# Kernel tuning notes

Measured on AMD Instinct MI355X. Metric: run time of the kernel, lower is better.

## Reference

```python
import jax, jax.numpy as jnp
import numpy as np

TOPK, NPRO, NALP, NADS = 13, 31, 24, 37
ALPHA, BETA, EPS = 1.0, 6.0, 1e-9
BS, NA, NM = 32, 8400, 64
IMG = 640.0


def _make_boxes(key, shape, img=IMG):
    k1, k2 = jax.random.split(key)
    cxy = jax.random.uniform(k1, shape[:-1] + (2,), minval=0.0, maxval=img)
    wh = jax.random.uniform(k2, shape[:-1] + (2,), minval=10.0, maxval=120.0)
    return jnp.concatenate([cxy - wh / 2, cxy + wh / 2], axis=-1)


def setup_inputs() -> dict:
    key = jax.random.key(0)
    ks = jax.random.split(key, 12)
    pd_pro_scores = jax.random.uniform(ks[0], (BS, NA, NPRO))
    pd_alp_scores = jax.random.uniform(ks[1], (BS, NA, NALP))
    pd_ads_scores = jax.random.uniform(ks[2], (5, BS, NA, NADS))
    pd_bboxes = _make_boxes(ks[3], (BS, NA, 4))
    pd_corners = jax.random.uniform(ks[4], (BS, NA, 8), maxval=IMG)
    anc_points = jax.random.uniform(ks[5], (NA, 2), maxval=IMG)
    gt_pro = jax.random.randint(ks[6], (BS, NM, 1), 0, NPRO, dtype=jnp.int32)
    gt_alp = jax.random.randint(ks[7], (BS, NM, 1), 0, NALP, dtype=jnp.int32)
    gt_ads = jax.random.randint(ks[8], (BS, NM, 5), 0, NADS, dtype=jnp.int32)
    gt_bboxes = _make_boxes(ks[9], (BS, NM, 4))
    gt_corners = jax.random.uniform(ks[10], (BS, NM, 8), maxval=IMG)
    nvalid = jax.random.randint(ks[11], (BS,), NM // 2, NM + 1)
    mask_gt = (jnp.arange(NM)[None, :] < nvalid[:, None]).astype(jnp.float32)[..., None]
    return {"pd_pro_scores": pd_pro_scores, "pd_alp_scores": pd_alp_scores,
            "pd_ads_scores": pd_ads_scores, "pd_bboxes": pd_bboxes,
            "pd_corners": pd_corners, "anc_points": anc_points,
            "gt_pro": gt_pro, "gt_alp": gt_alp, "gt_ads": gt_ads,
            "gt_bboxes": gt_bboxes, "gt_corners": gt_corners, "mask_gt": mask_gt}


def _iou(gt, pd):
    # gt: (bs, nm, 4) xyxy; pd: (bs, na, 4) xyxy -> (bs, nm, na)
    g, p = gt[:, :, None, :], pd[:, None, :, :]
    lt = jnp.maximum(g[..., :2], p[..., :2])
    rb = jnp.minimum(g[..., 2:], p[..., 2:])
    inter = jnp.clip(rb - lt, 0).prod(-1)
    a1 = jnp.clip(g[..., 2:] - g[..., :2], 0).prod(-1)
    a2 = jnp.clip(p[..., 2:] - p[..., :2], 0).prod(-1)
    return inter / (a1 + a2 - inter + EPS)


def reference(pd_pro_scores, pd_alp_scores, pd_ads_scores, pd_bboxes, pd_corners,
              anc_points, gt_pro, gt_alp, gt_ads, gt_bboxes, gt_corners, mask_gt):
    bs, na = pd_pro_scores.shape[:2]
    nm = gt_bboxes.shape[1]
    b = jnp.arange(bs)[:, None]

    # --- get_box_metrics ---
    labels = gt_pro[..., 0].astype(jnp.int32)                       # (bs, nm)
    bbox_scores = pd_pro_scores.transpose(0, 2, 1)[b, labels]       # (bs, nm, na)
    overlaps = _iou(gt_bboxes, pd_bboxes)                           # (bs, nm, na)
    align = (bbox_scores ** ALPHA) * (overlaps ** BETA)

    # --- select_candidates_in_gts ---
    xy = anc_points[None, None]                                     # (1,1,na,2)
    d_lt = xy - gt_bboxes[:, :, None, :2]
    d_rb = gt_bboxes[:, :, None, 2:] - xy
    mask_in = (jnp.minimum(d_lt, d_rb).min(-1) > EPS).astype(align.dtype)

    # --- select_topk_candidates ---
    metrics = align * mask_in
    _, tidx = jax.lax.top_k(metrics, TOPK)                          # (bs, nm, topk)
    valid = mask_gt[..., 0] > 0                                     # (bs, nm)
    tidx = jnp.where(valid[..., None], tidx, 0)
    rows = jnp.arange(bs * nm)[:, None]
    counts = jnp.zeros((bs * nm, na), jnp.int32).at[rows, tidx.reshape(bs * nm, TOPK)].add(1)
    counts = counts.reshape(bs, nm, na)
    is_in_topk = jnp.where(counts > 1, 0, counts).astype(metrics.dtype)
    mask_pos = is_in_topk * mask_in * mask_gt                       # (bs, nm, na)

    # --- select_highest_overlaps ---
    fg_mask = mask_pos.sum(-2)                                      # (bs, na)
    multi = fg_mask > 1
    max_idx = overlaps.argmax(1)                                    # (bs, na)
    is_max = (jnp.arange(nm)[None, :, None] == max_idx[:, None, :]).astype(mask_pos.dtype)
    mask_pos = jnp.where(multi[:, None, :], is_max, mask_pos)
    fg_mask = mask_pos.sum(-2)
    target_gt_idx = mask_pos.argmax(-2)                             # (bs, na)

    # --- get_targets ---
    target_pro = jnp.maximum(gt_pro[..., 0].astype(jnp.int32)[b, target_gt_idx], 0)
    target_alp = jnp.maximum(gt_alp[..., 0].astype(jnp.int32)[b, target_gt_idx], 0)
    target_ads = jnp.maximum(gt_ads.astype(jnp.int32)[b, target_gt_idx], 0)   # (bs, na, 5)
    target_ad0_4 = jnp.moveaxis(target_ads, -1, 0)                  # (5, bs, na)
    target_bboxes = gt_bboxes[b, target_gt_idx]                     # (bs, na, 4)
    target_corners = gt_corners[b, target_gt_idx]                   # (bs, na, 8)

    fg = (fg_mask > 0).astype(jnp.float32)                          # (bs, na)
    pro_scores = jax.nn.one_hot(target_pro, NPRO, dtype=jnp.float32) * fg[..., None]
    alp_scores = jax.nn.one_hot(target_alp, NALP, dtype=jnp.float32) * fg[..., None]
    ads_scores = jax.nn.one_hot(target_ad0_4, NADS, dtype=jnp.float32) * fg[None, :, :, None]

    # --- normalization of pro scores ---
    align = align * mask_pos
    pos_align = align.max(-1, keepdims=True)                        # (bs, nm, 1)
    pos_ov = (overlaps * mask_pos).max(-1, keepdims=True)           # (bs, nm, 1)
    norm = (align * pos_ov / (pos_align + EPS)).max(-2)[..., None]  # (bs, na, 1)
    pro_scores = pro_scores * norm

    return (target_pro, target_alp, target_ad0_4, target_bboxes, target_corners,
            pro_scores, alp_scores, ads_scores, fg_mask > 0)
```

## Files before the change

### kernel.cpp

```cpp
#include <hip/hip_runtime.h>
#include <cstdint>
#include <cstddef>

#define BS 32
#define NA 8400
#define NM 64
#define NPRO 31
#define NALP 24
#define NADS 37
#define TOPK 13
#define FEPS 1e-9f
#define WORDS 264
#define CAP 512
#define TL 16

#define OFF0 0L
#define OFF1 268800L
#define OFF2 537600L
#define OFF3 1881600L
#define OFF4 2956800L
#define OFF5 5107200L
#define OFF6 13440000L
#define OFF7 19891200L
#define OFF8 69619200L

__device__ __forceinline__ float iou1(float4 g, float ga, float4 p, float pa) {
  float iw = fmaxf(fminf(g.z, p.z) - fmaxf(g.x, p.x), 0.f);
  float ih = fmaxf(fminf(g.w, p.w) - fmaxf(g.y, p.y), 0.f);
  float inter = iw * ih;
  return inter / (ga + pa - inter + FEPS);
}

__global__ __launch_bounds__(256) void kA(
    const float* __restrict__ pro, const float* __restrict__ pd_bb,
    const float* __restrict__ anc, const int* __restrict__ gt_pro,
    const float* __restrict__ gt_bb, const float* __restrict__ mask_gt,
    short* __restrict__ tlist, unsigned* __restrict__ posA,
    unsigned* __restrict__ posO)
{
  __shared__ unsigned s_in[WORDS];
  __shared__ unsigned s_pos[WORDS];
  __shared__ float s_cv[CAP];
  __shared__ int   s_ci[CAP];
  __shared__ int   s_cnt;

  const int bm = blockIdx.x;
  const int b = bm >> 6;
  const int tid = threadIdx.x;
  const int lane = tid & 63;

  if (tid == 0) { posA[bm] = 0u; posO[bm] = 0u; s_cnt = 0; }

  short* tl = tlist + bm * TL;
  if (!(mask_gt[bm] > 0.f)) {
    if (tid == 0) tl[0] = 0;
    return;
  }
  __syncthreads();

  const float4 g = *(const float4*)(gt_bb + (size_t)bm * 4);
  const int label = gt_pro[bm];
  const float ga = fmaxf(g.z - g.x, 0.f) * fmaxf(g.w - g.y, 0.f);
  const float* pb = pd_bb + (size_t)b * NA * 4;
  const float* ps = pro + (size_t)b * NA * NPRO + label;

  for (int j = 0; j < (NA + 255) / 256; j++) {
    const int a = j * 256 + tid;
    bool inb = false, posb = false; float met = 0.f;
    if (a < NA) {
      float2 ap = *(const float2*)(anc + 2 * a);
      float din = fminf(fminf(ap.x - g.x, ap.y - g.y), fminf(g.z - ap.x, g.w - ap.y));
      if (din > FEPS) {
        inb = true;
        float4 p = *(const float4*)(pb + (size_t)a * 4);
        float pa = fmaxf(p.z - p.x, 0.f) * fmaxf(p.w - p.y, 0.f);
        float iou = iou1(g, ga, p, pa);
        float i2 = iou * iou;
        met = ps[(size_t)a * NPRO] * (i2 * i2 * i2);
        posb = met > 0.f;
      }
    }
    unsigned long long bin  = __ballot(inb);
    unsigned long long bpos = __ballot(posb);
    if (lane == 0) {
      int w0 = (j << 3) + ((tid >> 6) << 1);
      s_in[w0]      = (unsigned)bin;
      s_in[w0 + 1]  = (unsigned)(bin >> 32);
      s_pos[w0]     = (unsigned)bpos;
      s_pos[w0 + 1] = (unsigned)(bpos >> 32);
    }
    if (bpos) {
      int base = 0;
      if (lane == 0) base = atomicAdd(&s_cnt, __popcll(bpos));
      base = __shfl(base, 0);
      if (posb) {
        int idx = base + __popcll(bpos & ((1ull << lane) - 1ull));
        if (idx < CAP) { s_cv[idx] = met; s_ci[idx] = a; }
      }
    }
  }
  __syncthreads();

  const int P = min(s_cnt, CAP);
  if (tid < 64) {
    float lv[8]; int li[8];
#pragma unroll
    for (int e = 0; e < 8; e++) {
      int p = tid + e * 64;
      bool ok = p < P;
      lv[e] = ok ? s_cv[p] : -1.f;
      li[e] = ok ? s_ci[p] : NA;
    }
    const int nsel = min(P, TOPK);
    for (int k = 0; k < nsel; k++) {
      float bv = -1.f; int bi = NA;
#pragma unroll
      for (int e = 0; e < 8; e++)
        if (lv[e] > bv || (lv[e] == bv && li[e] < bi)) { bv = lv[e]; bi = li[e]; }
      for (int s = 1; s < 64; s <<= 1) {
        float ov = __shfl_xor(bv, s);
        int   oi = __shfl_xor(bi, s);
        if (ov > bv || (ov == bv && oi < bi)) { bv = ov; bi = oi; }
      }
#pragma unroll
      for (int e = 0; e < 8; e++) if (li[e] == bi) lv[e] = -1.f;
      if (tid == 0) tl[1 + k] = (short)bi;
    }
    if (tid == 0) {
      int cnt = nsel;
      if (P < TOPK) {
        int need = TOPK - P;
        for (int a = 0; a < NA && need > 0; a++) {
          if (!((s_pos[a >> 5] >> (a & 31)) & 1u)) {
            need--;
            if ((s_in[a >> 5] >> (a & 31)) & 1u) tl[1 + cnt++] = (short)a;
          }
        }
      }
      tl[0] = (short)cnt;
    }
  }
}

__global__ __launch_bounds__(256) void kB(
    const float* __restrict__ pro, const float* __restrict__ pd_bb,
    const int* __restrict__ gt_pro, const float* __restrict__ gt_bb,
    const short* __restrict__ tlist,
    unsigned* __restrict__ posA, unsigned* __restrict__ posO,
    int* __restrict__ tgi, float* __restrict__ fgo, float* __restrict__ avo)
{
  __shared__ float4 s_g[NM];
  __shared__ float s_ga[NM];
  __shared__ int s_lab[NM];
  __shared__ unsigned long long s_m[256];
  __shared__ short s_tl[NM * TL];

  const int b = blockIdx.y;
  const int a0 = blockIdx.x << 8;
  const int tid = threadIdx.x;

  s_m[tid] = 0ull;
  if (tid < NM) {
    float4 gg = *(const float4*)(gt_bb + (size_t)(b * NM + tid) * 4);
    s_g[tid] = gg;
    s_ga[tid] = fmaxf(gg.z - gg.x, 0.f) * fmaxf(gg.w - gg.y, 0.f);
    s_lab[tid] = gt_pro[b * NM + tid];
  }
  for (int i = tid; i < NM * TL / 2; i += 256)
    ((int*)s_tl)[i] = ((const int*)(tlist + (size_t)b * NM * TL))[i];
  __syncthreads();

  for (int i = tid; i < NM * TL; i += 256) {
    int m = i >> 4, sl = i & 15;
    if (sl >= 1 && sl <= (int)s_tl[m * TL]) {
      int ai = s_tl[i];
      unsigned d = (unsigned)(ai - a0);
      if (d < 256u) atomicOr(&s_m[d], 1ull << m);
    }
  }
  __syncthreads();

  const int a = a0 + tid;
  if (a >= NA) return;

  const int ia = b * NA + a;
  unsigned long long msk = s_m[tid];
  int cnt = __popcll(msk);
  int chosen = 0; float ovv = 0.f, av = 0.f, fg = 0.f;

  if (cnt > 0) {
    fg = 1.f;
    float4 p = *(const float4*)(pd_bb + (size_t)ia * 4);
    float pa = fmaxf(p.z - p.x, 0.f) * fmaxf(p.w - p.y, 0.f);
    if (cnt == 1) {
      chosen = __ffsll(msk) - 1;
      ovv = iou1(s_g[chosen], s_ga[chosen], p, pa);
    } else {
      float best = -1.f; int bmx = 0;
      for (int m = 0; m < NM; m++) {
        float v = iou1(s_g[m], s_ga[m], p, pa);
        if (v > best) { best = v; bmx = m; }
      }
      chosen = bmx; ovv = best;
    }
    float sc = pro[(size_t)ia * NPRO + s_lab[chosen]];
    float o2 = ovv * ovv;
    av = sc * (o2 * o2 * o2);
    atomicMax(&posA[b * NM + chosen], __float_as_uint(av));
    atomicMax(&posO[b * NM + chosen], __float_as_uint(ovv));
  }
  tgi[ia] = chosen; fgo[ia] = fg; avo[ia] = av;
}

__global__ __launch_bounds__(64) void kC(
    const int* __restrict__ gt_pro, const int* __restrict__ gt_alp,
    const int* __restrict__ gt_ads, const float* __restrict__ gt_bb,
    const float* __restrict__ gt_cor,
    const unsigned* __restrict__ posA, const unsigned* __restrict__ posO,
    const int* __restrict__ tgi, const float* __restrict__ fgi,
    const float* __restrict__ avi, float* __restrict__ out)
{
  __shared__ int s_tp[64], s_ta[64];
  __shared__ int s_td[5][64];
  __shared__ float s_pv[64], s_fg[64];

  const int b = blockIdx.y;
  const int a0 = blockIdx.x * 64;
  const int tid = threadIdx.x;
  const int na = min(64, NA - a0);
  const int a = a0 + tid;

  if (tid < na) {
    const int ia = b * NA + a;
    const int g = tgi[ia];
    const float fg = fgi[ia];
    float no = 0.f;
    if (fg > 0.f) {
      no = avi[ia] * __uint_as_float(posO[b * NM + g]) /
           (__uint_as_float(posA[b * NM + g]) + FEPS);
    }
    const int gi = b * NM + g;
    const int tp = gt_pro[gi], ta = gt_alp[gi];
    s_tp[tid] = tp; s_ta[tid] = ta; s_pv[tid] = no; s_fg[tid] = fg;
    out[OFF0 + ia] = (float)tp;
    out[OFF1 + ia] = (float)ta;
#pragma unroll
    for (int k = 0; k < 5; k++) {
      int td = gt_ads[(size_t)gi * 5 + k];
      s_td[k][tid] = td;
      out[OFF2 + (size_t)k * (BS * NA) + ia] = (float)td;
    }
    float4 bb = *(const float4*)(gt_bb + (size_t)gi * 4);
    *(float4*)(out + OFF3 + (size_t)ia * 4) = bb;
    float4 c0 = *(const float4*)(gt_cor + (size_t)gi * 8);
    float4 c1 = *(const float4*)(gt_cor + (size_t)gi * 8 + 4);
    *(float4*)(out + OFF4 + (size_t)ia * 8) = c0;
    *(float4*)(out + OFF4 + (size_t)ia * 8 + 4) = c1;
    out[OFF8 + ia] = fg;
  }
  __syncthreads();

  {
    float* dst = out + OFF5 + ((size_t)b * NA + a0) * NPRO;
    const int n = na * NPRO;
    for (int e4 = tid * 4; e4 < n; e4 += 256) {
      float vv[4];
#pragma unroll
      for (int j = 0; j < 4; j++) {
        int e = e4 + j; int al = e / NPRO; int c = e - al * NPRO;
        vv[j] = (c == s_tp[al]) ? s_pv[al] : 0.f;
      }
      *(float4*)(dst + e4) = make_float4(vv[0], vv[1], vv[2], vv[3]);
    }
  }
  {
    float* dst = out + OFF6 + ((size_t)b * NA + a0) * NALP;
    const int n = na * NALP;
    for (int e4 = tid * 4; e4 < n; e4 += 256) {
      float vv[4];
#pragma unroll
      for (int j = 0; j < 4; j++) {
        int e = e4 + j; int al = e / NALP; int c = e - al * NALP;
        vv[j] = (c == s_ta[al]) ? s_fg[al] : 0.f;
      }
      *(float4*)(dst + e4) = make_float4(vv[0], vv[1], vv[2], vv[3]);
    }
  }
#pragma unroll
  for (int k = 0; k < 5; k++) {
    float* dst = out + OFF7 + (size_t)k * ((size_t)BS * NA * NADS) +
                 ((size_t)b * NA + a0) * NADS;
    const int n = na * NADS;
    for (int e4 = tid * 4; e4 < n; e4 += 256) {
      float vv[4];
#pragma unroll
      for (int j = 0; j < 4; j++) {
        int e = e4 + j; int al = e / NADS; int c = e - al * NADS;
        vv[j] = (c == s_td[k][al]) ? s_fg[al] : 0.f;
      }
      *(float4*)(dst + e4) = make_float4(vv[0], vv[1], vv[2], vv[3]);
    }
  }
}

extern "C" void kernel_launch(void* const* d_in, const int* in_sizes, int n_in,
                              void* d_out, int out_size, void* d_ws, size_t ws_size,
                              hipStream_t stream) {
  const float* pd_pro  = (const float*)d_in[0];
  const float* pd_bb   = (const float*)d_in[3];
  const float* anc     = (const float*)d_in[5];
  const int*   gt_pro  = (const int*)d_in[6];
  const int*   gt_alp  = (const int*)d_in[7];
  const int*   gt_ads  = (const int*)d_in[8];
  const float* gt_bb   = (const float*)d_in[9];
  const float* gt_cor  = (const float*)d_in[10];
  const float* mask_gt = (const float*)d_in[11];
  float* out = (float*)d_out;

  char* ws = (char*)d_ws;
  short*    tlist = (short*)(ws);
  unsigned* posA  = (unsigned*)(ws + 65536);
  unsigned* posO  = (unsigned*)(ws + 73728);
  int*      tgi   = (int*)     (ws + 81920);
  float*    fgo   = (float*)   (ws + 1157120);
  float*    avo   = (float*)   (ws + 2232320);

  kA<<<BS * NM, 256, 0, stream>>>(pd_pro, pd_bb, anc, gt_pro, gt_bb, mask_gt,
                                  tlist, posA, posO);
  dim3 gridB((NA + 255) / 256, BS);
  kB<<<gridB, 256, 0, stream>>>(pd_pro, pd_bb, gt_pro, gt_bb, tlist,
                                posA, posO, tgi, fgo, avo);
  dim3 gridC((NA + 63) / 64, BS);
  kC<<<gridC, 64, 0, stream>>>(gt_pro, gt_alp, gt_ads, gt_bb, gt_cor,
                               posA, posO, tgi, fgo, avo, out);
}
```

Baseline: 121.1 us.

## Fuse three kernels into one cooperative persistent kernel with grid syncs

Merges the top-k candidate, assignment and output-scatter kernels into one cooperative kernel of 1024 blocks, with grid.sync between phases. Per-anchor assignment results stay in registers across the grid sync instead of going through workspace arrays, and the output phase uses 256-anchor tiles instead of 64. This removes two kernel launches and the intermediate global traffic. In exchange it adds grid-wide barrier cost, limits occupancy to the co-resident grid, and makes blocks loop over 2048 GT and 1056 tile work items.

```diff
diff --git a/kernel.cpp b/kernel.cpp
--- a/kernel.cpp
+++ b/kernel.cpp
@@ -1,6 +1,9 @@
 #include <hip/hip_runtime.h>
+#include <hip/hip_cooperative_groups.h>
 #include <cstdint>
 #include <cstddef>
+
+namespace cg = cooperative_groups;
 
 #define BS 32
 #define NA 8400
@@ -13,6 +16,8 @@
 #define WORDS 264
 #define CAP 512
 #define TL 16
+#define GRID 1024
+#define NTILE (BS * 33)
 
 #define OFF0 0L
 #define OFF1 268800L
@@ -31,274 +36,279 @@
   return inter / (ga + pa - inter + FEPS);
 }
 
-__global__ __launch_bounds__(256) void kA(
+__global__ __launch_bounds__(256, 4) void fused(
     const float* __restrict__ pro, const float* __restrict__ pd_bb,
     const float* __restrict__ anc, const int* __restrict__ gt_pro,
-    const float* __restrict__ gt_bb, const float* __restrict__ mask_gt,
+    const int* __restrict__ gt_alp, const int* __restrict__ gt_ads,
+    const float* __restrict__ gt_bb, const float* __restrict__ gt_cor,
+    const float* __restrict__ mask_gt,
     short* __restrict__ tlist, unsigned* __restrict__ posA,
-    unsigned* __restrict__ posO)
+    unsigned* __restrict__ posO, float* __restrict__ out)
 {
+  cg::grid_group grid = cg::this_grid();
+
   __shared__ unsigned s_in[WORDS];
   __shared__ unsigned s_pos[WORDS];
   __shared__ float s_cv[CAP];
   __shared__ int   s_ci[CAP];
   __shared__ int   s_cnt;
-
-  const int bm = blockIdx.x;
-  const int b = bm >> 6;
-  const int tid = threadIdx.x;
-  const int lane = tid & 63;
-
-  if (tid == 0) { posA[bm] = 0u; posO[bm] = 0u; s_cnt = 0; }
-
-  short* tl = tlist + bm * TL;
-  if (!(mask_gt[bm] > 0.f)) {
-    if (tid == 0) tl[0] = 0;
-    return;
-  }
-  __syncthreads();
-
-  const float4 g = *(const float4*)(gt_bb + (size_t)bm * 4);
-  const int label = gt_pro[bm];
-  const float ga = fmaxf(g.z - g.x, 0.f) * fmaxf(g.w - g.y, 0.f);
-  const float* pb = pd_bb + (size_t)b * NA * 4;
-  const float* ps = pro + (size_t)b * NA * NPRO + label;
-
-  for (int j = 0; j < (NA + 255) / 256; j++) {
-    const int a = j * 256 + tid;
-    bool inb = false, posb = false; float met = 0.f;
-    if (a < NA) {
-      float2 ap = *(const float2*)(anc + 2 * a);
-      float din = fminf(fminf(ap.x - g.x, ap.y - g.y), fminf(g.z - ap.x, g.w - ap.y));
-      if (din > FEPS) {
-        inb = true;
-        float4 p = *(const float4*)(pb + (size_t)a * 4);
-        float pa = fmaxf(p.z - p.x, 0.f) * fmaxf(p.w - p.y, 0.f);
-        float iou = iou1(g, ga, p, pa);
-        float i2 = iou * iou;
-        met = ps[(size_t)a * NPRO] * (i2 * i2 * i2);
-        posb = met > 0.f;
-      }
-    }
-    unsigned long long bin  = __ballot(inb);
-    unsigned long long bpos = __ballot(posb);
-    if (lane == 0) {
-      int w0 = (j << 3) + ((tid >> 6) << 1);
-      s_in[w0]      = (unsigned)bin;
-      s_in[w0 + 1]  = (unsigned)(bin >> 32);
-      s_pos[w0]     = (unsigned)bpos;
-      s_pos[w0 + 1] = (unsigned)(bpos >> 32);
-    }
-    if (bpos) {
-      int base = 0;
-      if (lane == 0) base = atomicAdd(&s_cnt, __popcll(bpos));
-      base = __shfl(base, 0);
-      if (posb) {
-        int idx = base + __popcll(bpos & ((1ull << lane) - 1ull));
-        if (idx < CAP) { s_cv[idx] = met; s_ci[idx] = a; }
-      }
-    }
-  }
-  __syncthreads();
-
-  const int P = min(s_cnt, CAP);
-  if (tid < 64) {
-    float lv[8]; int li[8];
-#pragma unroll
-    for (int e = 0; e < 8; e++) {
-      int p = tid + e * 64;
-      bool ok = p < P;
-      lv[e] = ok ? s_cv[p] : -1.f;
-      li[e] = ok ? s_ci[p] : NA;
-    }
-    const int nsel = min(P, TOPK);
-    for (int k = 0; k < nsel; k++) {
-      float bv = -1.f; int bi = NA;
-#pragma unroll
-      for (int e = 0; e < 8; e++)
-        if (lv[e] > bv || (lv[e] == bv && li[e] < bi)) { bv = lv[e]; bi = li[e]; }
-      for (int s = 1; s < 64; s <<= 1) {
-        float ov = __shfl_xor(bv, s);
-        int   oi = __shfl_xor(bi, s);
-        if (ov > bv || (ov == bv && oi < bi)) { bv = ov; bi = oi; }
-      }
-#pragma unroll
-      for (int e = 0; e < 8; e++) if (li[e] == bi) lv[e] = -1.f;
-      if (tid == 0) tl[1 + k] = (short)bi;
-    }
-    if (tid == 0) {
-      int cnt = nsel;
-      if (P < TOPK) {
-        int need = TOPK - P;
-        for (int a = 0; a < NA && need > 0; a++) {
-          if (!((s_pos[a >> 5] >> (a & 31)) & 1u)) {
-            need--;
-            if ((s_in[a >> 5] >> (a & 31)) & 1u) tl[1 + cnt++] = (short)a;
-          }
-        }
-      }
-      tl[0] = (short)cnt;
-    }
-  }
-}
-
-__global__ __launch_bounds__(256) void kB(
-    const float* __restrict__ pro, const float* __restrict__ pd_bb,
-    const int* __restrict__ gt_pro, const float* __restrict__ gt_bb,
-    const short* __restrict__ tlist,
-    unsigned* __restrict__ posA, unsigned* __restrict__ posO,
-    int* __restrict__ tgi, float* __restrict__ fgo, float* __restrict__ avo)
-{
   __shared__ float4 s_g[NM];
   __shared__ float s_ga[NM];
   __shared__ int s_lab[NM];
   __shared__ unsigned long long s_m[256];
   __shared__ short s_tl[NM * TL];
-
-  const int b = blockIdx.y;
-  const int a0 = blockIdx.x << 8;
+  __shared__ int s_tp[256], s_ta[256];
+  __shared__ int s_td[5][256];
+  __shared__ float s_pv[256], s_fg[256];
+
+  const int bid = blockIdx.x;
   const int tid = threadIdx.x;
-
-  s_m[tid] = 0ull;
-  if (tid < NM) {
-    float4 gg = *(const float4*)(gt_bb + (size_t)(b * NM + tid) * 4);
-    s_g[tid] = gg;
-    s_ga[tid] = fmaxf(gg.z - gg.x, 0.f) * fmaxf(gg.w - gg.y, 0.f);
-    s_lab[tid] = gt_pro[b * NM + tid];
+  const int lane = tid & 63;
+
+#pragma unroll
+  for (int gi = 0; gi < 2; gi++) {
+    const int bm = bid + gi * GRID;
+    const int b = bm >> 6;
+    const bool gvalid = (mask_gt[bm] > 0.f);
+    short* tl = tlist + bm * TL;
+    if (tid == 0) { posA[bm] = 0u; posO[bm] = 0u; s_cnt = 0; if (!gvalid) tl[0] = 0; }
+    __syncthreads();
+
+    if (gvalid) {
+      const float4 g = *(const float4*)(gt_bb + (size_t)bm * 4);
+      const int label = gt_pro[bm];
+      const float ga = fmaxf(g.z - g.x, 0.f) * fmaxf(g.w - g.y, 0.f);
+      const float* pb = pd_bb + (size_t)b * NA * 4;
+      const float* ps = pro + (size_t)b * NA * NPRO + label;
+
+      for (int j = 0; j < (NA + 255) / 256; j++) {
+        const int a = j * 256 + tid;
+        bool inb = false, posb = false; float met = 0.f;
+        if (a < NA) {
+          float2 ap = *(const float2*)(anc + 2 * a);
+          float din = fminf(fminf(ap.x - g.x, ap.y - g.y), fminf(g.z - ap.x, g.w - ap.y));
+          if (din > FEPS) {
+            inb = true;
+            float4 p = *(const float4*)(pb + (size_t)a * 4);
+            float pa = fmaxf(p.z - p.x, 0.f) * fmaxf(p.w - p.y, 0.f);
+            float iou = iou1(g, ga, p, pa);
+            float i2 = iou * iou;
+            met = ps[(size_t)a * NPRO] * (i2 * i2 * i2);
+            posb = met > 0.f;
+          }
+        }
+        unsigned long long bin  = __ballot(inb);
+        unsigned long long bpos = __ballot(posb);
+        if (lane == 0) {
+          int w0 = (j << 3) + ((tid >> 6) << 1);
+          s_in[w0]      = (unsigned)bin;
+          s_in[w0 + 1]  = (unsigned)(bin >> 32);
+          s_pos[w0]     = (unsigned)bpos;
+          s_pos[w0 + 1] = (unsigned)(bpos >> 32);
+        }
+        if (bpos) {
+          int base = 0;
+          if (lane == 0) base = atomicAdd(&s_cnt, __popcll(bpos));
+          base = __shfl(base, 0);
+          if (posb) {
+            int idx = base + __popcll(bpos & ((1ull << lane) - 1ull));
+            if (idx < CAP) { s_cv[idx] = met; s_ci[idx] = a; }
+          }
+        }
+      }
+    }
+    __syncthreads();
+
+    if (gvalid && tid < 64) {
+      const int P = min(s_cnt, CAP);
+      float lv[8]; int li[8];
+#pragma unroll
+      for (int e = 0; e < 8; e++) {
+        int p = tid + e * 64;
+        bool ok = p < P;
+        lv[e] = ok ? s_cv[p] : -1.f;
+        li[e] = ok ? s_ci[p] : NA;
+      }
+      const int nsel = min(P, TOPK);
+      for (int k = 0; k < nsel; k++) {
+        float bv = -1.f; int bi = NA;
+#pragma unroll
+        for (int e = 0; e < 8; e++)
+          if (lv[e] > bv || (lv[e] == bv && li[e] < bi)) { bv = lv[e]; bi = li[e]; }
+        for (int s = 1; s < 64; s <<= 1) {
+          float ov = __shfl_xor(bv, s);
+          int   oi = __shfl_xor(bi, s);
+          if (ov > bv || (ov == bv && oi < bi)) { bv = ov; bi = oi; }
+        }
+#pragma unroll
+        for (int e = 0; e < 8; e++) if (li[e] == bi) lv[e] = -1.f;
+        if (tid == 0) tl[1 + k] = (short)bi;
+      }
+      if (tid == 0) {
+        int cnt = nsel;
+        if (P < TOPK) {
+          int need = TOPK - P;
+          for (int a = 0; a < NA && need > 0; a++) {
+            if (!((s_pos[a >> 5] >> (a & 31)) & 1u)) {
+              need--;
+              if ((s_in[a >> 5] >> (a & 31)) & 1u) tl[1 + cnt++] = (short)a;
+            }
+          }
+        }
+        tl[0] = (short)cnt;
+      }
+    }
+    __syncthreads();
   }
-  for (int i = tid; i < NM * TL / 2; i += 256)
-    ((int*)s_tl)[i] = ((const int*)(tlist + (size_t)b * NM * TL))[i];
-  __syncthreads();
-
-  for (int i = tid; i < NM * TL; i += 256) {
-    int m = i >> 4, sl = i & 15;
-    if (sl >= 1 && sl <= (int)s_tl[m * TL]) {
-      int ai = s_tl[i];
-      unsigned d = (unsigned)(ai - a0);
-      if (d < 256u) atomicOr(&s_m[d], 1ull << m);
+
+  grid.sync();
+
+  int   ch_[2] = {0, 0};
+  float fg_[2] = {0.f, 0.f};
+  float av_[2] = {0.f, 0.f};
+#pragma unroll
+  for (int s = 0; s < 2; s++) {
+    const int t = bid + s * GRID;
+    if (t < NTILE) {
+      const int b = t / 33;
+      const int a0 = (t % 33) << 8;
+
+      s_m[tid] = 0ull;
+      if (tid < NM) {
+        float4 gg = *(const float4*)(gt_bb + (size_t)(b * NM + tid) * 4);
+        s_g[tid] = gg;
+        s_ga[tid] = fmaxf(gg.z - gg.x, 0.f) * fmaxf(gg.w - gg.y, 0.f);
+        s_lab[tid] = gt_pro[b * NM + tid];
+      }
+      for (int i = tid; i < NM * TL / 2; i += 256)
+        ((int*)s_tl)[i] = ((const int*)(tlist + (size_t)b * NM * TL))[i];
+      __syncthreads();
+
+      for (int i = tid; i < NM * TL; i += 256) {
+        int m = i >> 4, sl = i & 15;
+        if (sl >= 1 && sl <= (int)s_tl[m * TL]) {
+          int ai = s_tl[i];
+          unsigned d = (unsigned)(ai - a0);
+          if (d < 256u) atomicOr(&s_m[d], 1ull << m);
+        }
+      }
+      __syncthreads();
+
+      const int a = a0 + tid;
+      if (a < NA) {
+        const int ia = b * NA + a;
+        unsigned long long msk = s_m[tid];
+        int cnt = __popcll(msk);
+        if (cnt > 0) {
+          int chosen; float ovv;
+          float4 p = *(const float4*)(pd_bb + (size_t)ia * 4);
+          float pa = fmaxf(p.z - p.x, 0.f) * fmaxf(p.w - p.y, 0.f);
+          if (cnt == 1) {
+            chosen = __ffsll(msk) - 1;
+            ovv = iou1(s_g[chosen], s_ga[chosen], p, pa);
+          } else {
+            float best = -1.f; int bmx = 0;
+            for (int m = 0; m < NM; m++) {
+              float v = iou1(s_g[m], s_ga[m], p, pa);
+              if (v > best) { best = v; bmx = m; }
+            }
+            chosen = bmx; ovv = best;
+          }
+          float sc = pro[(size_t)ia * NPRO + s_lab[chosen]];
+          float o2 = ovv * ovv;
+          float av = sc * (o2 * o2 * o2);
+          ch_[s] = chosen; fg_[s] = 1.f; av_[s] = av;
+          atomicMax(&posA[b * NM + chosen], __float_as_uint(av));
+          atomicMax(&posO[b * NM + chosen], __float_as_uint(ovv));
+        }
+      }
+      __syncthreads();
     }
   }
-  __syncthreads();
-
-  const int a = a0 + tid;
-  if (a >= NA) return;
-
-  const int ia = b * NA + a;
-  unsigned long long msk = s_m[tid];
-  int cnt = __popcll(msk);
-  int chosen = 0; float ovv = 0.f, av = 0.f, fg = 0.f;
-
-  if (cnt > 0) {
-    fg = 1.f;
-    float4 p = *(const float4*)(pd_bb + (size_t)ia * 4);
-    float pa = fmaxf(p.z - p.x, 0.f) * fmaxf(p.w - p.y, 0.f);
-    if (cnt == 1) {
-      chosen = __ffsll(msk) - 1;
-      ovv = iou1(s_g[chosen], s_ga[chosen], p, pa);
-    } else {
-      float best = -1.f; int bmx = 0;
-      for (int m = 0; m < NM; m++) {
-        float v = iou1(s_g[m], s_ga[m], p, pa);
-        if (v > best) { best = v; bmx = m; }
-      }
-      chosen = bmx; ovv = best;
-    }
-    float sc = pro[(size_t)ia * NPRO + s_lab[chosen]];
-    float o2 = ovv * ovv;
-    av = sc * (o2 * o2 * o2);
-    atomicMax(&posA[b * NM + chosen], __float_as_uint(av));
-    atomicMax(&posO[b * NM + chosen], __float_as_uint(ovv));
-  }
-  tgi[ia] = chosen; fgo[ia] = fg; avo[ia] = av;
-}
-
-__global__ __launch_bounds__(64) void kC(
-    const int* __restrict__ gt_pro, const int* __restrict__ gt_alp,
-    const int* __restrict__ gt_ads, const float* __restrict__ gt_bb,
-    const float* __restrict__ gt_cor,
-    const unsigned* __restrict__ posA, const unsigned* __restrict__ posO,
-    const int* __restrict__ tgi, const float* __restrict__ fgi,
-    const float* __restrict__ avi, float* __restrict__ out)
-{
-  __shared__ int s_tp[64], s_ta[64];
-  __shared__ int s_td[5][64];
-  __shared__ float s_pv[64], s_fg[64];
-
-  const int b = blockIdx.y;
-  const int a0 = blockIdx.x * 64;
-  const int tid = threadIdx.x;
-  const int na = min(64, NA - a0);
-  const int a = a0 + tid;
-
-  if (tid < na) {
-    const int ia = b * NA + a;
-    const int g = tgi[ia];
-    const float fg = fgi[ia];
-    float no = 0.f;
-    if (fg > 0.f) {
-      no = avi[ia] * __uint_as_float(posO[b * NM + g]) /
-           (__uint_as_float(posA[b * NM + g]) + FEPS);
-    }
-    const int gi = b * NM + g;
-    const int tp = gt_pro[gi], ta = gt_alp[gi];
-    s_tp[tid] = tp; s_ta[tid] = ta; s_pv[tid] = no; s_fg[tid] = fg;
-    out[OFF0 + ia] = (float)tp;
-    out[OFF1 + ia] = (float)ta;
-#pragma unroll
-    for (int k = 0; k < 5; k++) {
-      int td = gt_ads[(size_t)gi * 5 + k];
-      s_td[k][tid] = td;
-      out[OFF2 + (size_t)k * (BS * NA) + ia] = (float)td;
-    }
-    float4 bb = *(const float4*)(gt_bb + (size_t)gi * 4);
-    *(float4*)(out + OFF3 + (size_t)ia * 4) = bb;
-    float4 c0 = *(const float4*)(gt_cor + (size_t)gi * 8);
-    float4 c1 = *(const float4*)(gt_cor + (size_t)gi * 8 + 4);
-    *(float4*)(out + OFF4 + (size_t)ia * 8) = c0;
-    *(float4*)(out + OFF4 + (size_t)ia * 8 + 4) = c1;
-    out[OFF8 + ia] = fg;
-  }
-  __syncthreads();
-
-  {
-    float* dst = out + OFF5 + ((size_t)b * NA + a0) * NPRO;
-    const int n = na * NPRO;
-    for (int e4 = tid * 4; e4 < n; e4 += 256) {
-      float vv[4];
-#pragma unroll
-      for (int j = 0; j < 4; j++) {
-        int e = e4 + j; int al = e / NPRO; int c = e - al * NPRO;
-        vv[j] = (c == s_tp[al]) ? s_pv[al] : 0.f;
-      }
-      *(float4*)(dst + e4) = make_float4(vv[0], vv[1], vv[2], vv[3]);
-    }
-  }
-  {
-    float* dst = out + OFF6 + ((size_t)b * NA + a0) * NALP;
-    const int n = na * NALP;
-    for (int e4 = tid * 4; e4 < n; e4 += 256) {
-      float vv[4];
-#pragma unroll
-      for (int j = 0; j < 4; j++) {
-        int e = e4 + j; int al = e / NALP; int c = e - al * NALP;
-        vv[j] = (c == s_ta[al]) ? s_fg[al] : 0.f;
-      }
-      *(float4*)(dst + e4) = make_float4(vv[0], vv[1], vv[2], vv[3]);
-    }
-  }
-#pragma unroll
-  for (int k = 0; k < 5; k++) {
-    float* dst = out + OFF7 + (size_t)k * ((size_t)BS * NA * NADS) +
-                 ((size_t)b * NA + a0) * NADS;
-    const int n = na * NADS;
-    for (int e4 = tid * 4; e4 < n; e4 += 256) {
-      float vv[4];
-#pragma unroll
-      for (int j = 0; j < 4; j++) {
-        int e = e4 + j; int al = e / NADS; int c = e - al * NADS;
-        vv[j] = (c == s_td[k][al]) ? s_fg[al] : 0.f;
-      }
-      *(float4*)(dst + e4) = make_float4(vv[0], vv[1], vv[2], vv[3]);
+
+  grid.sync();
+
+#pragma unroll
+  for (int s = 0; s < 2; s++) {
+    const int t = bid + s * GRID;
+    if (t < NTILE) {
+      const int b = t / 33;
+      const int a0 = (t % 33) << 8;
+      const int na = min(256, NA - a0);
+      const int a = a0 + tid;
+
+      if (tid < na) {
+        const int ia = b * NA + a;
+        const int g = ch_[s];
+        const float fg = fg_[s];
+        float no = 0.f;
+        if (fg > 0.f) {
+          no = av_[s] * __uint_as_float(posO[b * NM + g]) /
+               (__uint_as_float(posA[b * NM + g]) + FEPS);
+        }
+        const int gidx = b * NM + g;
+        const int tp = gt_pro[gidx], ta = gt_alp[gidx];
+        s_tp[tid] = tp; s_ta[tid] = ta; s_pv[tid] = no; s_fg[tid] = fg;
+        out[OFF0 + ia] = (float)tp;
+        out[OFF1 + ia] = (float)ta;
+#pragma unroll
+        for (int k = 0; k < 5; k++) {
+          int td = gt_ads[(size_t)gidx * 5 + k];
+          s_td[k][tid] = td;
+          out[OFF2 + (size_t)k * (BS * NA) + ia] = (float)td;
+        }
+        float4 bb = *(const float4*)(gt_bb + (size_t)gidx * 4);
+        *(float4*)(out + OFF3 + (size_t)ia * 4) = bb;
+        float4 c0 = *(const float4*)(gt_cor + (size_t)gidx * 8);
+        float4 c1 = *(const float4*)(gt_cor + (size_t)gidx * 8 + 4);
+        *(float4*)(out + OFF4 + (size_t)ia * 8) = c0;
+        *(float4*)(out + OFF4 + (size_t)ia * 8 + 4) = c1;
+        out[OFF8 + ia] = fg;
+      }
+      __syncthreads();
+
+      {
+        float* dst = out + OFF5 + ((size_t)b * NA + a0) * NPRO;
+        const int n = na * NPRO;
+        for (int e4 = tid * 4; e4 < n; e4 += 1024) {
+          float vv[4];
+#pragma unroll
+          for (int j = 0; j < 4; j++) {
+            int e = e4 + j; int al = e / NPRO; int c = e - al * NPRO;
+            vv[j] = (c == s_tp[al]) ? s_pv[al] : 0.f;
+          }
+          *(float4*)(dst + e4) = make_float4(vv[0], vv[1], vv[2], vv[3]);
+        }
+      }
+      {
+        float* dst = out + OFF6 + ((size_t)b * NA + a0) * NALP;
+        const int n = na * NALP;
+        for (int e4 = tid * 4; e4 < n; e4 += 1024) {
+          float vv[4];
+#pragma unroll
+          for (int j = 0; j < 4; j++) {
+            int e = e4 + j; int al = e / NALP; int c = e - al * NALP;
+            vv[j] = (c == s_ta[al]) ? s_fg[al] : 0.f;
+          }
+          *(float4*)(dst + e4) = make_float4(vv[0], vv[1], vv[2], vv[3]);
+        }
+      }
+#pragma unroll
+      for (int k = 0; k < 5; k++) {
+        float* dst = out + OFF7 + (size_t)k * ((size_t)BS * NA * NADS) +
+                     ((size_t)b * NA + a0) * NADS;
+        const int n = na * NADS;
+        for (int e4 = tid * 4; e4 < n; e4 += 1024) {
+          float vv[4];
+#pragma unroll
+          for (int j = 0; j < 4; j++) {
+            int e = e4 + j; int al = e / NADS; int c = e - al * NADS;
+            vv[j] = (c == s_td[k][al]) ? s_fg[al] : 0.f;
+          }
+          *(float4*)(dst + e4) = make_float4(vv[0], vv[1], vv[2], vv[3]);
+        }
+      }
+      __syncthreads();
     }
   }
 }
@@ -321,16 +331,12 @@
   short*    tlist = (short*)(ws);
   unsigned* posA  = (unsigned*)(ws + 65536);
   unsigned* posO  = (unsigned*)(ws + 73728);
-  int*      tgi   = (int*)     (ws + 81920);
-  float*    fgo   = (float*)   (ws + 1157120);
-  float*    avo   = (float*)   (ws + 2232320);
-
-  kA<<<BS * NM, 256, 0, stream>>>(pd_pro, pd_bb, anc, gt_pro, gt_bb, mask_gt,
-                                  tlist, posA, posO);
-  dim3 gridB((NA + 255) / 256, BS);
-  kB<<<gridB, 256, 0, stream>>>(pd_pro, pd_bb, gt_pro, gt_bb, tlist,
-                                posA, posO, tgi, fgo, avo);
-  dim3 gridC((NA + 63) / 64, BS);
-  kC<<<gridC, 64, 0, stream>>>(gt_pro, gt_alp, gt_ads, gt_bb, gt_cor,
-                               posA, posO, tgi, fgo, avo, out);
+
+  void* args[] = {
+    (void*)&pd_pro, (void*)&pd_bb, (void*)&anc, (void*)&gt_pro,
+    (void*)&gt_alp, (void*)&gt_ads, (void*)&gt_bb, (void*)&gt_cor,
+    (void*)&mask_gt, (void*)&tlist, (void*)&posA, (void*)&posO, (void*)&out
+  };
+  hipLaunchCooperativeKernel((const void*)fused, dim3(GRID), dim3(256),
+                             args, 0, stream);
 }
```

Result: slower. 362.1 us (+199.0%).

## Prefill outputs with background values in k1, then scatter only foreground anchors

Applied to the files above, without the earlier changes.

The dense output fill (zeros for the one-hot score tensors and gt index 0 defaults for the targets) moves into extra blocks of the first kernel, where it runs alongside the top-k selection. The second kernel now appends only foreground anchors to a compacted list via a global atomic counter. The third kernel walks that list and scatters the per-anchor targets and one-hot ones, so background anchors are no longer processed. The list capacity is fixed, so a foreground count above LCAP would silently drop entries. The atomic counter also adds contention.

```diff
diff --git a/kernel.cpp b/kernel.cpp
--- a/kernel.cpp
+++ b/kernel.cpp
@@ -13,6 +13,8 @@
 #define WORDS 264
 #define CAP 512
 #define TL 16
+#define NFILL 4096
+#define LCAP 32768
 
 #define OFF0 0L
 #define OFF1 268800L
@@ -23,6 +25,14 @@
 #define OFF6 13440000L
 #define OFF7 19891200L
 #define OFF8 69619200L
+#define N4TOT 17472000L
+#define S1_4  67200L
+#define S2_4  134400L
+#define S3_4  470400L
+#define S4_4  739200L
+#define Z4    1276800L
+
+typedef float f4_t __attribute__((ext_vector_type(4)));
 
 __device__ __forceinline__ float iou1(float4 g, float ga, float4 p, float pa) {
   float iw = fmaxf(fminf(g.z, p.z) - fmaxf(g.x, p.x), 0.f);
@@ -31,12 +41,15 @@
   return inter / (ga + pa - inter + FEPS);
 }
 
-__global__ __launch_bounds__(256) void kA(
+__global__ __launch_bounds__(256) void k1(
     const float* __restrict__ pro, const float* __restrict__ pd_bb,
     const float* __restrict__ anc, const int* __restrict__ gt_pro,
-    const float* __restrict__ gt_bb, const float* __restrict__ mask_gt,
+    const int* __restrict__ gt_alp, const int* __restrict__ gt_ads,
+    const float* __restrict__ gt_bb, const float* __restrict__ gt_cor,
+    const float* __restrict__ mask_gt,
     short* __restrict__ tlist, unsigned* __restrict__ posA,
-    unsigned* __restrict__ posO)
+    unsigned* __restrict__ posO, int* __restrict__ gcnt,
+    float* __restrict__ out)
 {
   __shared__ unsigned s_in[WORDS];
   __shared__ unsigned s_pos[WORDS];
@@ -44,11 +57,44 @@
   __shared__ int   s_ci[CAP];
   __shared__ int   s_cnt;
 
-  const int bm = blockIdx.x;
+  const int bid = blockIdx.x;
+  const int tid = threadIdx.x;
+
+  if (bid >= BS * NM) {
+    f4_t* o4 = (f4_t*)out;
+    const long stride = (long)NFILL * 256;
+    for (long f4 = (long)(bid - BS * NM) * 256 + tid; f4 < N4TOT; f4 += stride) {
+      f4_t v;
+      if (f4 >= Z4) {
+        v = (f4_t){0.f, 0.f, 0.f, 0.f};
+      } else if (f4 < S3_4) {
+        int b; float s;
+        if (f4 < S1_4) { b = (int)(f4 / 2100); s = (float)gt_pro[b * NM]; }
+        else if (f4 < S2_4) { b = (int)((f4 - S1_4) / 2100); s = (float)gt_alp[b * NM]; }
+        else {
+          long idx = f4 - S2_4;
+          int k = (int)(idx / 67200);
+          int b2 = (int)(idx - (long)k * 67200) / 2100;
+          b = b2; s = (float)gt_ads[b * NM * 5 + k];
+        }
+        v = (f4_t){s, s, s, s};
+      } else if (f4 < S4_4) {
+        int idx = (int)(f4 - S3_4); int b = idx / 8400;
+        v = *(const f4_t*)(gt_bb + (size_t)b * NM * 4);
+      } else {
+        int idx = (int)(f4 - S4_4); int b = idx / 16800; int par = idx & 1;
+        v = *((const f4_t*)(gt_cor + (size_t)b * NM * 8) + par);
+      }
+      o4[f4] = v;
+    }
+    return;
+  }
+
+  const int bm = bid;
   const int b = bm >> 6;
-  const int tid = threadIdx.x;
   const int lane = tid & 63;
 
+  if (bm == 0 && tid == 0) *gcnt = 0;
   if (tid == 0) { posA[bm] = 0u; posO[bm] = 0u; s_cnt = 0; }
 
   short* tl = tlist + bm * TL;
@@ -142,12 +188,12 @@
   }
 }
 
-__global__ __launch_bounds__(256) void kB(
+__global__ __launch_bounds__(256) void k2(
     const float* __restrict__ pro, const float* __restrict__ pd_bb,
     const int* __restrict__ gt_pro, const float* __restrict__ gt_bb,
     const short* __restrict__ tlist,
     unsigned* __restrict__ posA, unsigned* __restrict__ posO,
-    int* __restrict__ tgi, float* __restrict__ fgo, float* __restrict__ avo)
+    int* __restrict__ gcnt, int* __restrict__ lpack, float* __restrict__ lav)
 {
   __shared__ float4 s_g[NM];
   __shared__ float s_ga[NM];
@@ -186,121 +232,68 @@
   const int ia = b * NA + a;
   unsigned long long msk = s_m[tid];
   int cnt = __popcll(msk);
-  int chosen = 0; float ovv = 0.f, av = 0.f, fg = 0.f;
-
-  if (cnt > 0) {
-    fg = 1.f;
-    float4 p = *(const float4*)(pd_bb + (size_t)ia * 4);
-    float pa = fmaxf(p.z - p.x, 0.f) * fmaxf(p.w - p.y, 0.f);
-    if (cnt == 1) {
-      chosen = __ffsll(msk) - 1;
-      ovv = iou1(s_g[chosen], s_ga[chosen], p, pa);
-    } else {
-      float best = -1.f; int bmx = 0;
-      for (int m = 0; m < NM; m++) {
-        float v = iou1(s_g[m], s_ga[m], p, pa);
-        if (v > best) { best = v; bmx = m; }
-      }
-      chosen = bmx; ovv = best;
-    }
-    float sc = pro[(size_t)ia * NPRO + s_lab[chosen]];
-    float o2 = ovv * ovv;
-    av = sc * (o2 * o2 * o2);
-    atomicMax(&posA[b * NM + chosen], __float_as_uint(av));
-    atomicMax(&posO[b * NM + chosen], __float_as_uint(ovv));
-  }
-  tgi[ia] = chosen; fgo[ia] = fg; avo[ia] = av;
-}
-
-__global__ __launch_bounds__(64) void kC(
+  if (cnt == 0) return;
+
+  int chosen; float ovv;
+  float4 p = *(const float4*)(pd_bb + (size_t)ia * 4);
+  float pa = fmaxf(p.z - p.x, 0.f) * fmaxf(p.w - p.y, 0.f);
+  if (cnt == 1) {
+    chosen = __ffsll(msk) - 1;
+    ovv = iou1(s_g[chosen], s_ga[chosen], p, pa);
+  } else {
+    float best = -1.f; int bmx = 0;
+    for (int m = 0; m < NM; m++) {
+      float v = iou1(s_g[m], s_ga[m], p, pa);
+      if (v > best) { best = v; bmx = m; }
+    }
+    chosen = bmx; ovv = best;
+  }
+  float sc = pro[(size_t)ia * NPRO + s_lab[chosen]];
+  float o2 = ovv * ovv;
+  float av = sc * (o2 * o2 * o2);
+  atomicMax(&posA[b * NM + chosen], __float_as_uint(av));
+  atomicMax(&posO[b * NM + chosen], __float_as_uint(ovv));
+  int idx = atomicAdd(gcnt, 1);
+  if (idx < LCAP) { lpack[idx] = ia | (chosen << 19); lav[idx] = av; }
+}
+
+__global__ __launch_bounds__(256) void k3(
+    const int* __restrict__ gcnt, const int* __restrict__ lpack,
+    const float* __restrict__ lav,
+    const unsigned* __restrict__ posA, const unsigned* __restrict__ posO,
     const int* __restrict__ gt_pro, const int* __restrict__ gt_alp,
     const int* __restrict__ gt_ads, const float* __restrict__ gt_bb,
-    const float* __restrict__ gt_cor,
-    const unsigned* __restrict__ posA, const unsigned* __restrict__ posO,
-    const int* __restrict__ tgi, const float* __restrict__ fgi,
-    const float* __restrict__ avi, float* __restrict__ out)
+    const float* __restrict__ gt_cor, float* __restrict__ out)
 {
-  __shared__ int s_tp[64], s_ta[64];
-  __shared__ int s_td[5][64];
-  __shared__ float s_pv[64], s_fg[64];
-
-  const int b = blockIdx.y;
-  const int a0 = blockIdx.x * 64;
-  const int tid = threadIdx.x;
-  const int na = min(64, NA - a0);
-  const int a = a0 + tid;
-
-  if (tid < na) {
-    const int ia = b * NA + a;
-    const int g = tgi[ia];
-    const float fg = fgi[ia];
-    float no = 0.f;
-    if (fg > 0.f) {
-      no = avi[ia] * __uint_as_float(posO[b * NM + g]) /
-           (__uint_as_float(posA[b * NM + g]) + FEPS);
-    }
-    const int gi = b * NM + g;
-    const int tp = gt_pro[gi], ta = gt_alp[gi];
-    s_tp[tid] = tp; s_ta[tid] = ta; s_pv[tid] = no; s_fg[tid] = fg;
-    out[OFF0 + ia] = (float)tp;
-    out[OFF1 + ia] = (float)ta;
-#pragma unroll
-    for (int k = 0; k < 5; k++) {
-      int td = gt_ads[(size_t)gi * 5 + k];
-      s_td[k][tid] = td;
-      out[OFF2 + (size_t)k * (BS * NA) + ia] = (float)td;
-    }
-    float4 bb = *(const float4*)(gt_bb + (size_t)gi * 4);
-    *(float4*)(out + OFF3 + (size_t)ia * 4) = bb;
-    float4 c0 = *(const float4*)(gt_cor + (size_t)gi * 8);
-    float4 c1 = *(const float4*)(gt_cor + (size_t)gi * 8 + 4);
-    *(float4*)(out + OFF4 + (size_t)ia * 8) = c0;
-    *(float4*)(out + OFF4 + (size_t)ia * 8 + 4) = c1;
-    out[OFF8 + ia] = fg;
-  }
-  __syncthreads();
-
-  {
-    float* dst = out + OFF5 + ((size_t)b * NA + a0) * NPRO;
-    const int n = na * NPRO;
-    for (int e4 = tid * 4; e4 < n; e4 += 256) {
-      float vv[4];
-#pragma unroll
-      for (int j = 0; j < 4; j++) {
-        int e = e4 + j; int al = e / NPRO; int c = e - al * NPRO;
-        vv[j] = (c == s_tp[al]) ? s_pv[al] : 0.f;
-      }
-      *(float4*)(dst + e4) = make_float4(vv[0], vv[1], vv[2], vv[3]);
-    }
-  }
-  {
-    float* dst = out + OFF6 + ((size_t)b * NA + a0) * NALP;
-    const int n = na * NALP;
-    for (int e4 = tid * 4; e4 < n; e4 += 256) {
-      float vv[4];
-#pragma unroll
-      for (int j = 0; j < 4; j++) {
-        int e = e4 + j; int al = e / NALP; int c = e - al * NALP;
-        vv[j] = (c == s_ta[al]) ? s_fg[al] : 0.f;
-      }
-      *(float4*)(dst + e4) = make_float4(vv[0], vv[1], vv[2], vv[3]);
-    }
-  }
+  const int n = min(*gcnt, LCAP);
+  const int i = blockIdx.x * 256 + threadIdx.x;
+  if (i >= n) return;
+
+  const int pk = lpack[i];
+  const int ia = pk & ((1 << 19) - 1);
+  const int g = pk >> 19;
+  const float av = lav[i];
+  const int b = ia / NA;
+  const int gi = b * NM + g;
+
+  const float no = av * __uint_as_float(posO[gi]) /
+                   (__uint_as_float(posA[gi]) + FEPS);
+  const int tp = gt_pro[gi], ta = gt_alp[gi];
+
+  out[OFF0 + ia] = (float)tp;
+  out[OFF1 + ia] = (float)ta;
 #pragma unroll
   for (int k = 0; k < 5; k++) {
-    float* dst = out + OFF7 + (size_t)k * ((size_t)BS * NA * NADS) +
-                 ((size_t)b * NA + a0) * NADS;
-    const int n = na * NADS;
-    for (int e4 = tid * 4; e4 < n; e4 += 256) {
-      float vv[4];
-#pragma unroll
-      for (int j = 0; j < 4; j++) {
-        int e = e4 + j; int al = e / NADS; int c = e - al * NADS;
-        vv[j] = (c == s_td[k][al]) ? s_fg[al] : 0.f;
-      }
-      *(float4*)(dst + e4) = make_float4(vv[0], vv[1], vv[2], vv[3]);
-    }
-  }
+    int td = gt_ads[(size_t)gi * 5 + k];
+    out[OFF2 + (size_t)k * (BS * NA) + ia] = (float)td;
+    out[OFF7 + (size_t)k * ((size_t)BS * NA * NADS) + (size_t)ia * NADS + td] = 1.f;
+  }
+  *(float4*)(out + OFF3 + (size_t)ia * 4) = *(const float4*)(gt_bb + (size_t)gi * 4);
+  *(float4*)(out + OFF4 + (size_t)ia * 8) = *(const float4*)(gt_cor + (size_t)gi * 8);
+  *(float4*)(out + OFF4 + (size_t)ia * 8 + 4) = *(const float4*)(gt_cor + (size_t)gi * 8 + 4);
+  out[OFF5 + (size_t)ia * NPRO + tp] = no;
+  out[OFF6 + (size_t)ia * NALP + ta] = 1.f;
+  out[OFF8 + ia] = 1.f;
 }
 
 extern "C" void kernel_launch(void* const* d_in, const int* in_sizes, int n_in,
@@ -321,16 +314,17 @@
   short*    tlist = (short*)(ws);
   unsigned* posA  = (unsigned*)(ws + 65536);
   unsigned* posO  = (unsigned*)(ws + 73728);
-  int*      tgi   = (int*)     (ws + 81920);
-  float*    fgo   = (float*)   (ws + 1157120);
-  float*    avo   = (float*)   (ws + 2232320);
-
-  kA<<<BS * NM, 256, 0, stream>>>(pd_pro, pd_bb, anc, gt_pro, gt_bb, mask_gt,
-                                  tlist, posA, posO);
+  int*      gcnt  = (int*)     (ws + 81920);
+  int*      lpack = (int*)     (ws + 82048);
+  float*    lav   = (float*)   (ws + 213120);
+
+  k1<<<BS * NM + NFILL, 256, 0, stream>>>(pd_pro, pd_bb, anc, gt_pro, gt_alp,
+                                          gt_ads, gt_bb, gt_cor, mask_gt,
+                                          tlist, posA, posO, gcnt, out);
   dim3 gridB((NA + 255) / 256, BS);
-  kB<<<gridB, 256, 0, stream>>>(pd_pro, pd_bb, gt_pro, gt_bb, tlist,
-                                posA, posO, tgi, fgo, avo);
-  dim3 gridC((NA + 63) / 64, BS);
-  kC<<<gridC, 64, 0, stream>>>(gt_pro, gt_alp, gt_ads, gt_bb, gt_cor,
-                               posA, posO, tgi, fgo, avo, out);
-}
+  k2<<<gridB, 256, 0, stream>>>(pd_pro, pd_bb, gt_pro, gt_bb, tlist,
+                                posA, posO, gcnt, lpack, lav);
+  k3<<<(LCAP + 255) / 256, 256, 0, stream>>>(gcnt, lpack, lav, posA, posO,
+                                             gt_pro, gt_alp, gt_ads, gt_bb,
+                                             gt_cor, out);
+}
```

Result: slower. 141.2 us (+16.6%).
